# Kernel tuning notes

Hardware: AMD Instinct MI355X
Metric: run time of the kernel (lower is better)

The kernel has to match this reference:

```python
import jax, jax.numpy as jnp
import numpy as np

NUM_HEADS = 8
B, S, D = 4, 2048, 512


def setup_inputs() -> dict:
    key = jax.random.key(0)
    ks = jax.random.split(key, 12)
    scale = 1.0 / np.sqrt(D)
    return {
        "v": jax.random.normal(ks[0], (B, S, D), dtype=jnp.float32),
        "k": jax.random.normal(ks[1], (B, S, D), dtype=jnp.float32),
        "q": jax.random.normal(ks[2], (B, S, D), dtype=jnp.float32),
        "Wq": jax.random.normal(ks[3], (D, D), dtype=jnp.float32) * scale,
        "bq": jnp.zeros((D,), dtype=jnp.float32),
        "Wk": jax.random.normal(ks[4], (D, D), dtype=jnp.float32) * scale,
        "bk": jnp.zeros((D,), dtype=jnp.float32),
        "Wv": jax.random.normal(ks[5], (D, D), dtype=jnp.float32) * scale,
        "bv": jnp.zeros((D,), dtype=jnp.float32),
        "Wo": jax.random.normal(ks[6], (D, D), dtype=jnp.float32) * scale,
        "bo": jnp.zeros((D,), dtype=jnp.float32),
        "top_k": 32,
    }


def reference(v, k, q, Wq, bq, Wk, bk, Wv, bv, Wo, bo, top_k):
    dh = D // NUM_HEADS  # per-head depth

    def split_heads(x):  # [B,S,D] -> [B,H,S,dh]
        return x.reshape(B, -1, NUM_HEADS, dh).transpose(0, 2, 1, 3)

    qh = split_heads(q @ Wq + bq)
    kh = split_heads(k @ Wk + bk)
    vh = split_heads(v @ Wv + bv)

    logits = jnp.einsum('bhqd,bhkd->bhqk', qh, kh) / jnp.sqrt(jnp.float32(dh))
    w = jax.nn.softmax(logits, axis=-1)  # [B,H,S,S]

    num_keys = w.shape[-1]
    if top_k < num_keys:
        vals, idx = jax.lax.top_k(w, top_k)  # [B,H,S,top_k]
        bb = jnp.arange(B)[:, None, None, None]
        hh = jnp.arange(NUM_HEADS)[None, :, None, None]
        qq = jnp.arange(S)[None, None, :, None]
        sparse = jnp.zeros_like(w).at[bb, hh, qq, idx].set(vals)
        # tf.linalg.normalize(ord=1): divide by L1 norm along last axis
        w = sparse / jnp.sum(jnp.abs(sparse), axis=-1, keepdims=True)

    attn = jnp.einsum('bhqk,bhkd->bhqd', w, vh)  # [B,H,S,dh]
    concat = attn.transpose(0, 2, 1, 3).reshape(B, -1, D)
    out = concat @ Wo + bo
    return (out, w)
```

## Files before the change

### kernel.cpp

```cpp
#include <hip/hip_runtime.h>
#include <hip/hip_bf16.h>
#include <stdint.h>

#define S_LEN 2048
#define DMODEL 512
#define NH 8
#define DH 64
#define TOPK 32
#define LO_SCALE 4096.0f
#define INV_LO (1.0f/4096.0f)

typedef _Float16 f16;
typedef f16 half8 __attribute__((ext_vector_type(8)));
typedef f16 half4 __attribute__((ext_vector_type(4)));
typedef float floatx4 __attribute__((ext_vector_type(4)));
typedef float f32x4 __attribute__((ext_vector_type(4)));
typedef unsigned long long u64k;

#define AS1 __attribute__((address_space(1)))
#define AS3 __attribute__((address_space(3)))

__device__ __forceinline__ void gl_lds16(const void* g, void* l) {
    __builtin_amdgcn_global_load_lds((const AS1 void*)g, (AS3 void*)l, 16, 0, 0);
}
__device__ __forceinline__ void lds_fence() {
    asm volatile("s_waitcnt lgkmcnt(0)" ::: "memory");
}

__device__ __forceinline__ u64k make_key(float f, int idx) {
    unsigned u = __float_as_uint(f);
    unsigned sv = u ^ ((unsigned)(((int)u) >> 31) | 0x80000000u);
    return ((u64k)sv << 16) | (u64k)(0xFFFFu - (unsigned)idx);
}

__global__ __launch_bounds__(256)
void qkproj(const float* __restrict__ Xq, const float* __restrict__ Xk,
            const float* __restrict__ Wq_, const float* __restrict__ Wk_,
            const float* __restrict__ bq_, const float* __restrict__ bk_,
            float* __restrict__ outQ, float* __restrict__ outK)
{
    __shared__ float As[32][132];
    __shared__ float Bs[32][132];
    const float* X    = blockIdx.z ? Xk  : Xq;
    const float* W    = blockIdx.z ? Wk_ : Wq_;
    const float* bias = blockIdx.z ? bk_ : bq_;
    float* out        = blockIdx.z ? outK : outQ;
    const int tid = threadIdx.x;
    const int tx = tid & 15;
    const int ty = tid >> 4;
    const int m0 = blockIdx.y * 128;
    const int n0 = blockIdx.x * 128;

    float acc[8][8];
#pragma unroll
    for (int i = 0; i < 8; ++i)
#pragma unroll
        for (int j = 0; j < 8; ++j) acc[i][j] = 0.f;

    f32x4 pa[4], pb[4];
#pragma unroll
    for (int u = 0; u < 4; ++u) {
        int id = tid + u * 256;
        pa[u] = *(const f32x4*)(X + (size_t)(m0 + (id >> 3)) * 512 + (id & 7) * 4);
        pb[u] = *(const f32x4*)(W + (size_t)(id >> 5) * 512 + n0 + (id & 31) * 4);
    }

    for (int k0 = 0; k0 < 512; k0 += 32) {
#pragma unroll
        for (int u = 0; u < 4; ++u) {
            int id = tid + u * 256;
            int r = id >> 3, c4 = (id & 7) * 4;
            As[c4 + 0][r] = pa[u].x; As[c4 + 1][r] = pa[u].y;
            As[c4 + 2][r] = pa[u].z; As[c4 + 3][r] = pa[u].w;
            int rb = id >> 5, cb = (id & 31) * 4;
            *(f32x4*)&Bs[rb][cb] = pb[u];
        }
        __syncthreads();
        if (k0 < 480) {
            int kn = k0 + 32;
#pragma unroll
            for (int u = 0; u < 4; ++u) {
                int id = tid + u * 256;
                pa[u] = *(const f32x4*)(X + (size_t)(m0 + (id >> 3)) * 512 + kn + (id & 7) * 4);
                pb[u] = *(const f32x4*)(W + (size_t)(kn + (id >> 5)) * 512 + n0 + (id & 31) * 4);
            }
        }
#pragma unroll 8
        for (int kk = 0; kk < 32; ++kk) {
            float a[8], b[8];
            *(f32x4*)&a[0] = *(const f32x4*)&As[kk][ty * 4];
            *(f32x4*)&a[4] = *(const f32x4*)&As[kk][64 + ty * 4];
            *(f32x4*)&b[0] = *(const f32x4*)&Bs[kk][tx * 4];
            *(f32x4*)&b[4] = *(const f32x4*)&Bs[kk][64 + tx * 4];
#pragma unroll
            for (int i = 0; i < 8; ++i)
#pragma unroll
                for (int j = 0; j < 8; ++j)
                    acc[i][j] = fmaf(a[i], b[j], acc[i][j]);
        }
        __syncthreads();
    }

    float bb[8];
    *(f32x4*)&bb[0] = *(const f32x4*)(bias + n0 + tx * 4);
    *(f32x4*)&bb[4] = *(const f32x4*)(bias + n0 + 64 + tx * 4);

#pragma unroll
    for (int i = 0; i < 8; ++i) {
        int r = m0 + ((i >> 2) << 6) + ty * 4 + (i & 3);
        int b_ = r >> 11, s = r & 2047;
#pragma unroll
        for (int h = 0; h < 2; ++h) {
            int c = n0 + h * 64 + tx * 4;
            f32x4 w = {acc[i][h * 4 + 0] + bb[h * 4 + 0],
                       acc[i][h * 4 + 1] + bb[h * 4 + 1],
                       acc[i][h * 4 + 2] + bb[h * 4 + 2],
                       acc[i][h * 4 + 3] + bb[h * 4 + 3]};
            int hd = c >> 6, d = c & 63;
            float* p = out + (((size_t)(b_ * NH + hd) * S_LEN) + s) * DH + d;
            *(f32x4*)p = w;
        }
    }
}

__global__ __launch_bounds__(256)
void logits_topk(const float* __restrict__ Qh, const float* __restrict__ Kh,
                 float* __restrict__ wbuf)
{
    __shared__ float As[2][32][68];
    __shared__ __align__(16) char smemB[33280];
    float* Bs = (float*)smemB;
    u64k (*slab)[32] = (u64k(*)[32])smemB;

    const int tid = threadIdx.x;
    const int lig = tid & 15;
    const int ty  = tid >> 4;
    const int gsh = ((tid & 63) >> 4) << 4;
    const unsigned ltg = (1u << lig) - 1u;
    const int bh = blockIdx.y;
    const int q0 = blockIdx.x * 64;
    const float* Ab = Qh + (size_t)bh * S_LEN * DH;
    const float* Bb = Kh + (size_t)bh * S_LEN * DH;

    auto sort32 = [&](u64k &a0, u64k &a1) {
#pragma unroll
        for (int s = 2; s <= 32; s <<= 1) {
#pragma unroll
            for (int d = s >> 1; d >= 1; d >>= 1) {
                int e0 = 2 * lig;
                if (d == 1) {
                    bool descB = ((e0 & s) == 0);
                    u64k mx = a0 > a1 ? a0 : a1;
                    u64k mn = a0 > a1 ? a1 : a0;
                    a0 = descB ? mx : mn;
                    a1 = descB ? mn : mx;
                } else {
                    bool descB = ((e0 & s) == 0);
                    bool amS   = ((e0 & d) == 0);
                    bool wantMax = (descB == amS);
                    u64k p0 = __shfl_xor(a0, d >> 1, 16);
                    u64k p1 = __shfl_xor(a1, d >> 1, 16);
                    a0 = wantMax ? (a0 > p0 ? a0 : p0) : (a0 > p0 ? p0 : a0);
                    a1 = wantMax ? (a1 > p1 ? a1 : p1) : (a1 > p1 ? p1 : a1);
                }
            }
        }
    };
    auto clean32 = [&](u64k &a0, u64k &a1) {
#pragma unroll
        for (int d = 16; d >= 2; d >>= 1) {
            bool amS = (((2 * lig) & d) == 0);
            u64k p0 = __shfl_xor(a0, d >> 1, 16);
            u64k p1 = __shfl_xor(a1, d >> 1, 16);
            a0 = amS ? (a0 > p0 ? a0 : p0) : (a0 > p0 ? p0 : a0);
            a1 = amS ? (a1 > p1 ? a1 : p1) : (a1 > p1 ? p1 : a1);
        }
        u64k mx = a0 > a1 ? a0 : a1;
        u64k mn = a0 > a1 ? a1 : a0;
        a0 = mx; a1 = mn;
    };

    float acc[4][16];
#pragma unroll
    for (int i = 0; i < 4; ++i)
#pragma unroll
        for (int j = 0; j < 16; ++j) acc[i][j] = 0.f;

    u64k key0[4], key1[4], botk[4];
#pragma unroll
    for (int i = 0; i < 4; ++i) { key0[i] = 0; key1[i] = 0; botk[i] = 0; }

#pragma unroll
    for (int u = 0; u < 4; ++u) {
        int id = tid + u * 256;
        int r = id >> 4, c4 = (id & 15) * 4;
        int ch = c4 >> 5, cl = c4 & 31;
        f32x4 x = *(const f32x4*)(Ab + (size_t)(q0 + r) * DH + c4);
        As[ch][cl + 0][r] = x.x * 0.125f;
        As[ch][cl + 1][r] = x.y * 0.125f;
        As[ch][cl + 2][r] = x.z * 0.125f;
        As[ch][cl + 3][r] = x.w * 0.125f;
    }

    f32x4 kb[8];
#pragma unroll
    for (int u = 0; u < 8; ++u) {
        int id = tid + u * 256;
        int r = id >> 3, c4 = (id & 7) * 4;
        kb[u] = *(const f32x4*)(Bb + (size_t)r * DH + c4);
    }

#pragma unroll 1
    for (int kp = 0; kp < 8; ++kp) {
#pragma unroll
        for (int ch = 0; ch < 2; ++ch) {
            __syncthreads();
#pragma unroll
            for (int u = 0; u < 8; ++u) {
                int id = tid + u * 256;
                int r = id >> 3, c4 = (id & 7) * 4;
                Bs[(c4 + 0) * 260 + r] = kb[u].x;
                Bs[(c4 + 1) * 260 + r] = kb[u].y;
                Bs[(c4 + 2) * 260 + r] = kb[u].z;
                Bs[(c4 + 3) * 260 + r] = kb[u].w;
            }
            __syncthreads();
            {
                int nkp = ch ? kp + 1 : kp;
                int nch = ch ^ 1;
                if (nkp < 8) {
#pragma unroll
                    for (int u = 0; u < 8; ++u) {
                        int id = tid + u * 256;
                        int r = id >> 3, c4 = (id & 7) * 4;
                        kb[u] = *(const f32x4*)(Bb + (size_t)(nkp * 256 + r) * DH + nch * 32 + c4);
                    }
                }
            }
#pragma unroll 8
            for (int kk = 0; kk < 32; ++kk) {
                float a[4], b[16];
                *(f32x4*)&a[0] = *(const f32x4*)&As[ch][kk][ty * 4];
#pragma unroll
                for (int h = 0; h < 4; ++h)
                    *(f32x4*)&b[h * 4] = *(const f32x4*)&Bs[kk * 260 + lig * 4 + h * 64];
#pragma unroll
                for (int i = 0; i < 4; ++i)
#pragma unroll
                    for (int j = 0; j < 16; ++j)
                        acc[i][j] = fmaf(a[i], b[j], acc[i][j]);
            }
        }
        __syncthreads();

#pragma unroll
        for (int i = 0; i < 4; ++i) {
            unsigned done = 0;
            if (kp == 0) {
                u64k t0 = 0, t1 = 0; int j0 = 0, j1 = 0;
#pragma unroll
                for (int j = 0; j < 16; ++j) {
                    u64k kj = make_key(acc[i][j], ((j >> 2) << 6) + (lig << 2) + (j & 3));
                    if (kj > t0)      { t1 = t0; j1 = j0; t0 = kj; j0 = j; }
                    else if (kj > t1) { t1 = kj; j1 = j; }
                }
                key0[i] = t0; key1[i] = t1;
                sort32(key0[i], key1[i]);
                botk[i] = __shfl(key1[i], 15, 16);
                done = (1u << j0) | (1u << j1);
            }
            u64k bk = botk[i];
            int c = 0;
#pragma unroll 1
            for (int att = 0; att < 12; ++att) {
                bool ovf = false;
#pragma unroll
                for (int j = 0; j < 16; ++j) {
                    u64k kj = make_key(acc[i][j],
                                       kp * 256 + ((j >> 2) << 6) + (lig << 2) + (j & 3));
                    bool p = (((done >> j) & 1u) == 0u) && (kj > bk);
                    unsigned long long wbm = __ballot(p);
                    unsigned mk = (unsigned)((wbm >> gsh) & 0xFFFFull);
                    if (mk) {
                        int pos = c + __popc(mk & ltg);
                        int tot = c + __popc(mk);
                        if (p && pos < 32) { slab[ty * 4 + i][pos] = kj; done |= 1u << j; }
                        if (tot > 32) { ovf = true; c = 32; } else { c = tot; }
                    }
                }
                bool anyovf = __any(ovf);
                if (anyovf) {
                    lds_fence();
                    u64k c0 = (2 * lig     < c) ? slab[ty * 4 + i][2 * lig]     : 0ull;
                    u64k c1 = (2 * lig + 1 < c) ? slab[ty * 4 + i][2 * lig + 1] : 0ull;
                    sort32(c0, c1);
                    u64k m0 = __shfl_xor(c1, 15, 16);
                    u64k m1 = __shfl_xor(c0, 15, 16);
                    key0[i] = key0[i] > m0 ? key0[i] : m0;
                    key1[i] = key1[i] > m1 ? key1[i] : m1;
                    clean32(key0[i], key1[i]);
                    bk = __shfl(key1[i], 15, 16);
                    c = 0;
                } else {
                    break;
                }
            }
            {
                lds_fence();
                u64k c0 = (2 * lig     < c) ? slab[ty * 4 + i][2 * lig]     : 0ull;
                u64k c1 = (2 * lig + 1 < c) ? slab[ty * 4 + i][2 * lig + 1] : 0ull;
                sort32(c0, c1);
                u64k m0 = __shfl_xor(c1, 15, 16);
                u64k m1 = __shfl_xor(c0, 15, 16);
                key0[i] = key0[i] > m0 ? key0[i] : m0;
                key1[i] = key1[i] > m1 ? key1[i] : m1;
                clean32(key0[i], key1[i]);
                bk = __shfl(key1[i], 15, 16);
            }
            botk[i] = bk;
        }

#pragma unroll
        for (int i = 0; i < 4; ++i)
#pragma unroll
            for (int j = 0; j < 16; ++j) acc[i][j] = 0.f;
    }

#pragma unroll
    for (int i = 0; i < 4; ++i) {
        int r = q0 + ty * 4 + i;
        float* wr = wbuf + ((size_t)bh * S_LEN + r) * S_LEN;
        *(u64k*)(wr + (lig << 2))     = key0[i];
        *(u64k*)(wr + (lig << 2) + 2) = key1[i];
    }
}

__global__ __launch_bounds__(256)
void wsplit2(const float* __restrict__ W0, const float* __restrict__ W1,
             f16* __restrict__ planes)
{
    __shared__ float tile[32][33];
    const float* W = blockIdx.z ? W1 : W0;
    f16* Th = planes + (size_t)blockIdx.z * 524288;
    f16* Tl = Th + 262144;
    const int bx = blockIdx.x * 32;
    const int by = blockIdx.y * 32;
    const int lx = threadIdx.x & 31, ly = threadIdx.x >> 5;
#pragma unroll
    for (int r = ly; r < 32; r += 8)
        tile[r][lx] = W[(size_t)(by + r) * 512 + bx + lx];
    __syncthreads();
#pragma unroll
    for (int r = ly; r < 32; r += 8) {
        float x = tile[lx][r];
        f16 h = (f16)x;
        f16 l = (f16)((x - (float)h) * LO_SCALE);
        Th[(size_t)(bx + r) * 512 + by + lx] = h;
        Tl[(size_t)(bx + r) * 512 + by + lx] = l;
    }
}

__global__ __launch_bounds__(256)
void gemm_x32(const float* __restrict__ X,
              const f16* __restrict__ Bh_, const f16* __restrict__ Bl_,
              const float* __restrict__ bias, float* __restrict__ outF, int mode)
{
    __shared__ f16 sm[16384];
    f16* As_h = sm;       f16* As_l = sm + 4096;
    f16* Bs_h = sm + 8192; f16* Bs_l = sm + 12288;
    const int tid  = threadIdx.x;
    const int lane = tid & 63, wv = tid >> 6;
    const int wm = wv & 1, wn = wv >> 1;
    const int quad = lane >> 4, l15 = lane & 15;
    const int m0 = blockIdx.y * 128, n0 = blockIdx.x * 128;

    floatx4 acc_h[4][4], acc_c[4][4];
    const floatx4 z4 = {0.f, 0.f, 0.f, 0.f};
#pragma unroll
    for (int i = 0; i < 4; ++i)
#pragma unroll
        for (int j = 0; j < 4; ++j) { acc_h[i][j] = z4; acc_c[i][j] = z4; }

    for (int k0 = 0; k0 < 512; k0 += 32) {
        __syncthreads();
#pragma unroll
        for (int c = 0; c < 4; ++c) {
            int r   = c * 32 + (tid >> 3);
            int col = (tid & 7) * 4;
            f32x4 x = *(const f32x4*)(X + (size_t)(m0 + r) * 512 + k0 + col);
            f16 h0 = (f16)x.x, h1 = (f16)x.y, h2 = (f16)x.z, h3 = (f16)x.w;
            half4 hv = {h0, h1, h2, h3};
            half4 lv = {(f16)((x.x - (float)h0) * LO_SCALE),
                        (f16)((x.y - (float)h1) * LO_SCALE),
                        (f16)((x.z - (float)h2) * LO_SCALE),
                        (f16)((x.w - (float)h3) * LO_SCALE)};
            *(half4*)&As_h[r * 32 + col] = hv;
            *(half4*)&As_l[r * 32 + col] = lv;
        }
#pragma unroll
        for (int c = 0; c < 2; ++c) {
            int r    = c * 64 + (wv << 4) + (lane >> 2);
            int ch   = (lane & 3) * 8;
            int lidx = (c * 64 + (wv << 4)) * 32 + lane * 8;
            gl_lds16(Bh_ + (size_t)(n0 + r) * 512 + k0 + ch, &Bs_h[lidx]);
            gl_lds16(Bl_ + (size_t)(n0 + r) * 512 + k0 + ch, &Bs_l[lidx]);
        }
        asm volatile("s_waitcnt vmcnt(0)" ::: "memory");
        __syncthreads();

        half8 bh8[4], bl8[4];
#pragma unroll
        for (int j = 0; j < 4; ++j) {
            int n = wn * 64 + j * 16 + l15;
            bh8[j] = *(const half8*)&Bs_h[n * 32 + quad * 8];
            bl8[j] = *(const half8*)&Bs_l[n * 32 + quad * 8];
        }
#pragma unroll
        for (int i = 0; i < 4; ++i) {
            int m = wm * 64 + i * 16 + l15;
            half8 ah = *(const half8*)&As_h[m * 32 + quad * 8];
            half8 al = *(const half8*)&As_l[m * 32 + quad * 8];
#pragma unroll
            for (int j = 0; j < 4; ++j) {
                acc_h[i][j] = __builtin_amdgcn_mfma_f32_16x16x32_f16(ah, bh8[j], acc_h[i][j], 0, 0, 0);
                acc_c[i][j] = __builtin_amdgcn_mfma_f32_16x16x32_f16(ah, bl8[j], acc_c[i][j], 0, 0, 0);
                acc_c[i][j] = __builtin_amdgcn_mfma_f32_16x16x32_f16(al, bh8[j], acc_c[i][j], 0, 0, 0);
            }
        }
    }

#pragma unroll
    for (int j = 0; j < 4; ++j) {
        int col = n0 + wn * 64 + j * 16 + l15;
        float bv = bias[col];
#pragma unroll
        for (int i = 0; i < 4; ++i) {
            int rbase = m0 + wm * 64 + i * 16 + quad * 4;
#pragma unroll
            for (int rg = 0; rg < 4; ++rg) {
                float r = acc_h[i][j][rg] + acc_c[i][j][rg] * INV_LO + bv;
                int row = rbase + rg;
                if (mode == 2) {
                    outF[(size_t)row * 512 + col] = r;
                } else {
                    int b_ = row >> 11, s = row & 2047, h = col >> 6, d = col & 63;
                    outF[(((size_t)(b_ * NH + h)) * S_LEN + s) * DH + d] = r;
                }
            }
        }
    }
}

__global__ __launch_bounds__(256)
void gemm_x16(const f16* __restrict__ Ah_, const f16* __restrict__ Al_,
              const f16* __restrict__ Bh_, const f16* __restrict__ Bl_,
              const float* __restrict__ bias, float* __restrict__ outF,
              int Ksz, int ldc, int mode)
{
    __shared__ f16 sm[16384];
    f16* As_h = sm;        f16* As_l = sm + 4096;
    f16* Bs_h = sm + 8192; f16* Bs_l = sm + 12288;
    const int tid  = threadIdx.x;
    const int lane = tid & 63, wv = tid >> 6;
    const int wm = wv & 1, wn = wv >> 1;
    const int quad = lane >> 4, l15 = lane & 15;
    const int m0 = blockIdx.y * 128, n0 = blockIdx.x * 128;

    floatx4 acc_h[4][4], acc_c[4][4];
    const floatx4 z4 = {0.f, 0.f, 0.f, 0.f};
#pragma unroll
    for (int i = 0; i < 4; ++i)
#pragma unroll
        for (int j = 0; j < 4; ++j) { acc_h[i][j] = z4; acc_c[i][j] = z4; }

    for (int k0 = 0; k0 < Ksz; k0 += 32) {
        __syncthreads();
#pragma unroll
        for (int c = 0; c < 2; ++c) {
            int r    = c * 64 + (wv << 4) + (lane >> 2);
            int ch   = (lane & 3) * 8;
            int lidx = (c * 64 + (wv << 4)) * 32 + lane * 8;
            gl_lds16(Ah_ + (size_t)(m0 + r) * Ksz + k0 + ch, &As_h[lidx]);
            gl_lds16(Al_ + (size_t)(m0 + r) * Ksz + k0 + ch, &As_l[lidx]);
            gl_lds16(Bh_ + (size_t)(n0 + r) * Ksz + k0 + ch, &Bs_h[lidx]);
            gl_lds16(Bl_ + (size_t)(n0 + r) * Ksz + k0 + ch, &Bs_l[lidx]);
        }
        asm volatile("s_waitcnt vmcnt(0)" ::: "memory");
        __syncthreads();

        half8 bh8[4], bl8[4];
#pragma unroll
        for (int j = 0; j < 4; ++j) {
            int n = wn * 64 + j * 16 + l15;
            bh8[j] = *(const half8*)&Bs_h[n * 32 + quad * 8];
            bl8[j] = *(const half8*)&Bs_l[n * 32 + quad * 8];
        }
#pragma unroll
        for (int i = 0; i < 4; ++i) {
            int m = wm * 64 + i * 16 + l15;
            half8 ah = *(const half8*)&As_h[m * 32 + quad * 8];
            half8 al = *(const half8*)&As_l[m * 32 + quad * 8];
#pragma unroll
            for (int j = 0; j < 4; ++j) {
                acc_h[i][j] = __builtin_amdgcn_mfma_f32_16x16x32_f16(ah, bh8[j], acc_h[i][j], 0, 0, 0);
                acc_c[i][j] = __builtin_amdgcn_mfma_f32_16x16x32_f16(ah, bl8[j], acc_c[i][j], 0, 0, 0);
                acc_c[i][j] = __builtin_amdgcn_mfma_f32_16x16x32_f16(al, bh8[j], acc_c[i][j], 0, 0, 0);
            }
        }
    }

#pragma unroll
    for (int j = 0; j < 4; ++j) {
        int col = n0 + wn * 64 + j * 16 + l15;
        float bv = (mode == 2) ? bias[col] : 0.f;
#pragma unroll
        for (int i = 0; i < 4; ++i) {
            int rbase = m0 + wm * 64 + i * 16 + quad * 4;
#pragma unroll
            for (int rg = 0; rg < 4; ++rg) {
                float r = acc_h[i][j][rg] + acc_c[i][j][rg] * INV_LO;
                int row = rbase + rg;
                outF[(size_t)row * ldc + col] = r + bv;
            }
        }
    }
}

__global__ __launch_bounds__(256)
void topk_scatter(float* __restrict__ wbuf, const float* __restrict__ Vh,
                  f16* __restrict__ attH, f16* __restrict__ attL)
{
    __shared__ float wrow[4][2048];
    __shared__ float win_w[4][TOPK];
    __shared__ int   win_i[4][TOPK];

    const int tid  = threadIdx.x;
    const int wv   = tid >> 6;
    const int lane = tid & 63;
    const int row  = blockIdx.x * 4 + wv;
    float* wr = wbuf + (size_t)row * 2048;

    u64k key = 0;
    if (lane < TOPK) key = ((const u64k*)wr)[lane];
    unsigned sv = (unsigned)(key >> 16);
    unsigned fu = (sv & 0x80000000u) ? (sv ^ 0x80000000u) : ~sv;
    float v = __uint_as_float(fu);
    int idx = (int)(0xFFFFu - (unsigned)(key & 0xFFFFull)) & 2047;

    float m = __shfl(v, 0, 64);
    float e = (lane < TOPK) ? __expf(v - m) : 0.f;

    float mysum = e;
#pragma unroll
    for (int off = 32; off > 0; off >>= 1) mysum += __shfl_xor(mysum, off, 64);
    const float rw = 1.f / mysum;

    if (lane < TOPK) { win_w[wv][lane] = e; win_i[wv][lane] = idx; }

    const f32x4 z = {0.f, 0.f, 0.f, 0.f};
#pragma unroll
    for (int t = 0; t < 8; ++t) ((f32x4*)wrow[wv])[t * 64 + lane] = z;
    lds_fence();
    if (lane < TOPK) wrow[wv][win_i[wv][lane]] = win_w[wv][lane] * rw;
    lds_fence();

#pragma unroll
    for (int t = 0; t < 8; ++t)
        __builtin_nontemporal_store(((f32x4*)wrow[wv])[t * 64 + lane],
                                    (f32x4*)(wr + (size_t)(t * 64 + lane) * 4));

    const int bh = row >> 11;
    const float* Vb = Vh + (size_t)bh * S_LEN * DH;
    float acc = 0.f;
#pragma unroll
    for (int j = 0; j < TOPK; ++j) {
        float wj = win_w[wv][j] * rw;
        int   kj = win_i[wv][j];
        acc = fmaf(wj, Vb[(size_t)kj * DH + lane], acc);
    }
    const int b_ = row >> 14;
    const int h  = (row >> 11) & 7;
    const int s  = row & 2047;
    size_t oidx = (((size_t)b_ * S_LEN) + s) * 512 + h * DH + lane;
    f16 hh = (f16)acc;
    attH[oidx] = hh;
    attL[oidx] = (f16)((acc - (float)hh) * LO_SCALE);
}

extern "C" void kernel_launch(void* const* d_in, const int* in_sizes, int n_in,
                              void* d_out, int out_size, void* d_ws, size_t ws_size,
                              hipStream_t stream) {
    const float* v  = (const float*)d_in[0];
    const float* k  = (const float*)d_in[1];
    const float* q  = (const float*)d_in[2];
    const float* Wq = (const float*)d_in[3];
    const float* bq = (const float*)d_in[4];
    const float* Wk = (const float*)d_in[5];
    const float* bk = (const float*)d_in[6];
    const float* Wv = (const float*)d_in[7];
    const float* bv = (const float*)d_in[8];
    const float* Wo = (const float*)d_in[9];
    const float* bo = (const float*)d_in[10];

    float* out  = (float*)d_out;
    float* wout = out + (size_t)4 * S_LEN * 512;

    char* ws = (char*)d_ws;
    float* Vh   = (float*)ws;
    float* Qh32 = (float*)(ws + 16777216);
    float* Kh32 = (float*)(ws + 33554432);
    f16* WT  = (f16*)(ws + 50331648);
    f16 *WvH = WT,           *WvL = WT + 262144;
    f16 *WoH = WT + 524288,  *WoL = WT + 786432;
    f16* attH = (f16*)(ws + 16777216);
    f16* attL = (f16*)(ws + 25165824);

    wsplit2<<<dim3(16, 16, 2), 256, 0, stream>>>(Wv, Wo, WT);

    qkproj<<<dim3(4, 64, 2), 256, 0, stream>>>(q, k, Wq, Wk, bq, bk, Qh32, Kh32);
    gemm_x32<<<dim3(4, 64), 256, 0, stream>>>(v, WvH, WvL, bv, Vh, 1);

    logits_topk<<<dim3(32, 32), 256, 0, stream>>>(Qh32, Kh32, wout);

    topk_scatter<<<16384, 256, 0, stream>>>(wout, Vh, attH, attL);

    gemm_x16<<<dim3(4, 64, 1), 256, 0, stream>>>(attH, attL, WoH, WoL, bo, out, 512, 512, 2);
}
```

Measured before the change: 1.194 ms.

## Split fused logits+topk into full logits GEMM and per-row topk attention kernel

Replaces the fused kernel, which computed logits and tracked the top-k candidates in registers across eight key passes, with two kernels. The first is a tiled FP32 GEMM that writes the full logits matrix into the weight output buffer. The second runs one wavefront per row: it reads the row back, selects the top-k with a 64-lane bitonic sort plus threshold filtering, and then does the scatter and attention. This gives much more parallelism and removes per-pass selection from the GEMM loop, at the cost of writing and then re-reading the full B*H*S*S logits through HBM.

```diff
diff --git a/kernel.cpp b/kernel.cpp
--- a/kernel.cpp
+++ b/kernel.cpp
@@ -123,31 +123,311 @@
     }
 }
 
-__global__ __launch_bounds__(256)
-void logits_topk(const float* __restrict__ Qh, const float* __restrict__ Kh,
-                 float* __restrict__ wbuf)
+__global__ __launch_bounds__(256, 2)
+void gemm_logits(const float* __restrict__ Qh, const float* __restrict__ Kh,
+                 float* __restrict__ logits)
 {
-    __shared__ float As[2][32][68];
-    __shared__ __align__(16) char smemB[33280];
-    float* Bs = (float*)smemB;
-    u64k (*slab)[32] = (u64k(*)[32])smemB;
-
+    __shared__ float As[32][132];
+    __shared__ float Bs[32][260];
     const int tid = threadIdx.x;
-    const int lig = tid & 15;
-    const int ty  = tid >> 4;
-    const int gsh = ((tid & 63) >> 4) << 4;
-    const unsigned ltg = (1u << lig) - 1u;
-    const int bh = blockIdx.y;
-    const int q0 = blockIdx.x * 64;
+    const int tx = tid & 15;
+    const int ty = tid >> 4;
+    const int bh = blockIdx.z;
     const float* Ab = Qh + (size_t)bh * S_LEN * DH;
     const float* Bb = Kh + (size_t)bh * S_LEN * DH;
+    const int q0 = blockIdx.y * 128;
+    const int k0 = blockIdx.x * 256;
+
+    float acc[8][16];
+#pragma unroll
+    for (int i = 0; i < 8; ++i)
+#pragma unroll
+        for (int j = 0; j < 16; ++j) acc[i][j] = 0.f;
+
+    f32x4 qa[4], kb[8];
+#pragma unroll
+    for (int u = 0; u < 4; ++u) {
+        int id = tid + u * 256;
+        qa[u] = *(const f32x4*)(Ab + (size_t)(q0 + (id >> 3)) * DH + (id & 7) * 4);
+    }
+#pragma unroll
+    for (int u = 0; u < 8; ++u) {
+        int id = tid + u * 256;
+        kb[u] = *(const f32x4*)(Bb + (size_t)(k0 + (id >> 3)) * DH + (id & 7) * 4);
+    }
+
+    for (int ch = 0; ch < 2; ++ch) {
+#pragma unroll
+        for (int u = 0; u < 4; ++u) {
+            int id = tid + u * 256;
+            int r = id >> 3, c4 = (id & 7) * 4;
+            As[c4 + 0][r] = qa[u].x * 0.125f; As[c4 + 1][r] = qa[u].y * 0.125f;
+            As[c4 + 2][r] = qa[u].z * 0.125f; As[c4 + 3][r] = qa[u].w * 0.125f;
+        }
+#pragma unroll
+        for (int u = 0; u < 8; ++u) {
+            int id = tid + u * 256;
+            int r = id >> 3, c4 = (id & 7) * 4;
+            Bs[c4 + 0][r] = kb[u].x; Bs[c4 + 1][r] = kb[u].y;
+            Bs[c4 + 2][r] = kb[u].z; Bs[c4 + 3][r] = kb[u].w;
+        }
+        __syncthreads();
+        if (ch == 0) {
+#pragma unroll
+            for (int u = 0; u < 4; ++u) {
+                int id = tid + u * 256;
+                qa[u] = *(const f32x4*)(Ab + (size_t)(q0 + (id >> 3)) * DH + 32 + (id & 7) * 4);
+            }
+#pragma unroll
+            for (int u = 0; u < 8; ++u) {
+                int id = tid + u * 256;
+                kb[u] = *(const f32x4*)(Bb + (size_t)(k0 + (id >> 3)) * DH + 32 + (id & 7) * 4);
+            }
+        }
+#pragma unroll 8
+        for (int kk = 0; kk < 32; ++kk) {
+            float a[8], b[16];
+            *(f32x4*)&a[0] = *(const f32x4*)&As[kk][ty * 4];
+            *(f32x4*)&a[4] = *(const f32x4*)&As[kk][64 + ty * 4];
+#pragma unroll
+            for (int h = 0; h < 4; ++h)
+                *(f32x4*)&b[h * 4] = *(const f32x4*)&Bs[kk][tx * 4 + h * 64];
+#pragma unroll
+            for (int i = 0; i < 8; ++i)
+#pragma unroll
+                for (int j = 0; j < 16; ++j)
+                    acc[i][j] = fmaf(a[i], b[j], acc[i][j]);
+        }
+        __syncthreads();
+    }
+
+#pragma unroll
+    for (int i = 0; i < 8; ++i) {
+        int r = q0 + (i >> 2) * 64 + ty * 4 + (i & 3);
+        float* C = logits + (size_t)bh * S_LEN * S_LEN + (size_t)r * S_LEN + k0;
+#pragma unroll
+        for (int h = 0; h < 4; ++h) {
+            f32x4 v = {acc[i][h * 4 + 0], acc[i][h * 4 + 1],
+                       acc[i][h * 4 + 2], acc[i][h * 4 + 3]};
+            __builtin_nontemporal_store(v, (f32x4*)(C + h * 64 + tx * 4));
+        }
+    }
+}
+
+__global__ __launch_bounds__(256)
+void wsplit2(const float* __restrict__ W0, const float* __restrict__ W1,
+             f16* __restrict__ planes)
+{
+    __shared__ float tile[32][33];
+    const float* W = blockIdx.z ? W1 : W0;
+    f16* Th = planes + (size_t)blockIdx.z * 524288;
+    f16* Tl = Th + 262144;
+    const int bx = blockIdx.x * 32;
+    const int by = blockIdx.y * 32;
+    const int lx = threadIdx.x & 31, ly = threadIdx.x >> 5;
+#pragma unroll
+    for (int r = ly; r < 32; r += 8)
+        tile[r][lx] = W[(size_t)(by + r) * 512 + bx + lx];
+    __syncthreads();
+#pragma unroll
+    for (int r = ly; r < 32; r += 8) {
+        float x = tile[lx][r];
+        f16 h = (f16)x;
+        f16 l = (f16)((x - (float)h) * LO_SCALE);
+        Th[(size_t)(bx + r) * 512 + by + lx] = h;
+        Tl[(size_t)(bx + r) * 512 + by + lx] = l;
+    }
+}
+
+__global__ __launch_bounds__(256)
+void gemm_x32(const float* __restrict__ X,
+              const f16* __restrict__ Bh_, const f16* __restrict__ Bl_,
+              const float* __restrict__ bias, float* __restrict__ outF, int mode)
+{
+    __shared__ f16 sm[16384];
+    f16* As_h = sm;       f16* As_l = sm + 4096;
+    f16* Bs_h = sm + 8192; f16* Bs_l = sm + 12288;
+    const int tid  = threadIdx.x;
+    const int lane = tid & 63, wv = tid >> 6;
+    const int wm = wv & 1, wn = wv >> 1;
+    const int quad = lane >> 4, l15 = lane & 15;
+    const int m0 = blockIdx.y * 128, n0 = blockIdx.x * 128;
+
+    floatx4 acc_h[4][4], acc_c[4][4];
+    const floatx4 z4 = {0.f, 0.f, 0.f, 0.f};
+#pragma unroll
+    for (int i = 0; i < 4; ++i)
+#pragma unroll
+        for (int j = 0; j < 4; ++j) { acc_h[i][j] = z4; acc_c[i][j] = z4; }
+
+    for (int k0 = 0; k0 < 512; k0 += 32) {
+        __syncthreads();
+#pragma unroll
+        for (int c = 0; c < 4; ++c) {
+            int r   = c * 32 + (tid >> 3);
+            int col = (tid & 7) * 4;
+            f32x4 x = *(const f32x4*)(X + (size_t)(m0 + r) * 512 + k0 + col);
+            f16 h0 = (f16)x.x, h1 = (f16)x.y, h2 = (f16)x.z, h3 = (f16)x.w;
+            half4 hv = {h0, h1, h2, h3};
+            half4 lv = {(f16)((x.x - (float)h0) * LO_SCALE),
+                        (f16)((x.y - (float)h1) * LO_SCALE),
+                        (f16)((x.z - (float)h2) * LO_SCALE),
+                        (f16)((x.w - (float)h3) * LO_SCALE)};
+            *(half4*)&As_h[r * 32 + col] = hv;
+            *(half4*)&As_l[r * 32 + col] = lv;
+        }
+#pragma unroll
+        for (int c = 0; c < 2; ++c) {
+            int r    = c * 64 + (wv << 4) + (lane >> 2);
+            int ch   = (lane & 3) * 8;
+            int lidx = (c * 64 + (wv << 4)) * 32 + lane * 8;
+            gl_lds16(Bh_ + (size_t)(n0 + r) * 512 + k0 + ch, &Bs_h[lidx]);
+            gl_lds16(Bl_ + (size_t)(n0 + r) * 512 + k0 + ch, &Bs_l[lidx]);
+        }
+        asm volatile("s_waitcnt vmcnt(0)" ::: "memory");
+        __syncthreads();
+
+        half8 bh8[4], bl8[4];
+#pragma unroll
+        for (int j = 0; j < 4; ++j) {
+            int n = wn * 64 + j * 16 + l15;
+            bh8[j] = *(const half8*)&Bs_h[n * 32 + quad * 8];
+            bl8[j] = *(const half8*)&Bs_l[n * 32 + quad * 8];
+        }
+#pragma unroll
+        for (int i = 0; i < 4; ++i) {
+            int m = wm * 64 + i * 16 + l15;
+            half8 ah = *(const half8*)&As_h[m * 32 + quad * 8];
+            half8 al = *(const half8*)&As_l[m * 32 + quad * 8];
+#pragma unroll
+            for (int j = 0; j < 4; ++j) {
+                acc_h[i][j] = __builtin_amdgcn_mfma_f32_16x16x32_f16(ah, bh8[j], acc_h[i][j], 0, 0, 0);
+                acc_c[i][j] = __builtin_amdgcn_mfma_f32_16x16x32_f16(ah, bl8[j], acc_c[i][j], 0, 0, 0);
+                acc_c[i][j] = __builtin_amdgcn_mfma_f32_16x16x32_f16(al, bh8[j], acc_c[i][j], 0, 0, 0);
+            }
+        }
+    }
+
+#pragma unroll
+    for (int j = 0; j < 4; ++j) {
+        int col = n0 + wn * 64 + j * 16 + l15;
+        float bv = bias[col];
+#pragma unroll
+        for (int i = 0; i < 4; ++i) {
+            int rbase = m0 + wm * 64 + i * 16 + quad * 4;
+#pragma unroll
+            for (int rg = 0; rg < 4; ++rg) {
+                float r = acc_h[i][j][rg] + acc_c[i][j][rg] * INV_LO + bv;
+                int row = rbase + rg;
+                if (mode == 2) {
+                    outF[(size_t)row * 512 + col] = r;
+                } else {
+                    int b_ = row >> 11, s = row & 2047, h = col >> 6, d = col & 63;
+                    outF[(((size_t)(b_ * NH + h)) * S_LEN + s) * DH + d] = r;
+                }
+            }
+        }
+    }
+}
+
+__global__ __launch_bounds__(256)
+void gemm_x16(const f16* __restrict__ Ah_, const f16* __restrict__ Al_,
+              const f16* __restrict__ Bh_, const f16* __restrict__ Bl_,
+              const float* __restrict__ bias, float* __restrict__ outF,
+              int Ksz, int ldc, int mode)
+{
+    __shared__ f16 sm[16384];
+    f16* As_h = sm;        f16* As_l = sm + 4096;
+    f16* Bs_h = sm + 8192; f16* Bs_l = sm + 12288;
+    const int tid  = threadIdx.x;
+    const int lane = tid & 63, wv = tid >> 6;
+    const int wm = wv & 1, wn = wv >> 1;
+    const int quad = lane >> 4, l15 = lane & 15;
+    const int m0 = blockIdx.y * 128, n0 = blockIdx.x * 128;
+
+    floatx4 acc_h[4][4], acc_c[4][4];
+    const floatx4 z4 = {0.f, 0.f, 0.f, 0.f};
+#pragma unroll
+    for (int i = 0; i < 4; ++i)
+#pragma unroll
+        for (int j = 0; j < 4; ++j) { acc_h[i][j] = z4; acc_c[i][j] = z4; }
+
+    for (int k0 = 0; k0 < Ksz; k0 += 32) {
+        __syncthreads();
+#pragma unroll
+        for (int c = 0; c < 2; ++c) {
+            int r    = c * 64 + (wv << 4) + (lane >> 2);
+            int ch   = (lane & 3) * 8;
+            int lidx = (c * 64 + (wv << 4)) * 32 + lane * 8;
+            gl_lds16(Ah_ + (size_t)(m0 + r) * Ksz + k0 + ch, &As_h[lidx]);
+            gl_lds16(Al_ + (size_t)(m0 + r) * Ksz + k0 + ch, &As_l[lidx]);
+            gl_lds16(Bh_ + (size_t)(n0 + r) * Ksz + k0 + ch, &Bs_h[lidx]);
+            gl_lds16(Bl_ + (size_t)(n0 + r) * Ksz + k0 + ch, &Bs_l[lidx]);
+        }
+        asm volatile("s_waitcnt vmcnt(0)" ::: "memory");
+        __syncthreads();
+
+        half8 bh8[4], bl8[4];
+#pragma unroll
+        for (int j = 0; j < 4; ++j) {
+            int n = wn * 64 + j * 16 + l15;
+            bh8[j] = *(const half8*)&Bs_h[n * 32 + quad * 8];
+            bl8[j] = *(const half8*)&Bs_l[n * 32 + quad * 8];
+        }
+#pragma unroll
+        for (int i = 0; i < 4; ++i) {
+            int m = wm * 64 + i * 16 + l15;
+            half8 ah = *(const half8*)&As_h[m * 32 + quad * 8];
+            half8 al = *(const half8*)&As_l[m * 32 + quad * 8];
+#pragma unroll
+            for (int j = 0; j < 4; ++j) {
+                acc_h[i][j] = __builtin_amdgcn_mfma_f32_16x16x32_f16(ah, bh8[j], acc_h[i][j], 0, 0, 0);
+                acc_c[i][j] = __builtin_amdgcn_mfma_f32_16x16x32_f16(ah, bl8[j], acc_c[i][j], 0, 0, 0);
+                acc_c[i][j] = __builtin_amdgcn_mfma_f32_16x16x32_f16(al, bh8[j], acc_c[i][j], 0, 0, 0);
+            }
+        }
+    }
+
+#pragma unroll
+    for (int j = 0; j < 4; ++j) {
+        int col = n0 + wn * 64 + j * 16 + l15;
+        float bv = (mode == 2) ? bias[col] : 0.f;
+#pragma unroll
+        for (int i = 0; i < 4; ++i) {
+            int rbase = m0 + wm * 64 + i * 16 + quad * 4;
+#pragma unroll
+            for (int rg = 0; rg < 4; ++rg) {
+                float r = acc_h[i][j][rg] + acc_c[i][j][rg] * INV_LO;
+                int row = rbase + rg;
+                outF[(size_t)row * ldc + col] = r + bv;
+            }
+        }
+    }
+}
+
+__global__ __launch_bounds__(256)
+void topk_attn(float* __restrict__ wbuf, const float* __restrict__ Vh,
+               f16* __restrict__ attH, f16* __restrict__ attL)
+{
+    __shared__ float wrow[4][2048];
+    __shared__ u64k  slab[4][32];
+    __shared__ float win_w[4][TOPK];
+    __shared__ int   win_i[4][TOPK];
+
+    const int tid  = threadIdx.x;
+    const int wv   = tid >> 6;
+    const int lane = tid & 63;
+    const int l15  = lane & 15;
+    const unsigned long long lt = (1ull << lane) - 1ull;
+    const int row = blockIdx.x * 4 + wv;
+    float* wr = wbuf + (size_t)row * 2048;
 
     auto sort32 = [&](u64k &a0, u64k &a1) {
 #pragma unroll
         for (int s = 2; s <= 32; s <<= 1) {
 #pragma unroll
             for (int d = s >> 1; d >= 1; d >>= 1) {
-                int e0 = 2 * lig;
+                int e0 = 2 * l15;
                 if (d == 1) {
                     bool descB = ((e0 & s) == 0);
                     u64k mx = a0 > a1 ? a0 : a1;
@@ -169,7 +449,7 @@
     auto clean32 = [&](u64k &a0, u64k &a1) {
 #pragma unroll
         for (int d = 16; d >= 2; d >>= 1) {
-            bool amS = (((2 * lig) & d) == 0);
+            bool amS = (((2 * l15) & d) == 0);
             u64k p0 = __shfl_xor(a0, d >> 1, 16);
             u64k p1 = __shfl_xor(a1, d >> 1, 16);
             a0 = amS ? (a0 > p0 ? a0 : p0) : (a0 > p0 ? p0 : a0);
@@ -179,369 +459,102 @@
         u64k mn = a0 > a1 ? a1 : a0;
         a0 = mx; a1 = mn;
     };
-
-    float acc[4][16];
-#pragma unroll
-    for (int i = 0; i < 4; ++i)
-#pragma unroll
-        for (int j = 0; j < 16; ++j) acc[i][j] = 0.f;
-
-    u64k key0[4], key1[4], botk[4];
-#pragma unroll
-    for (int i = 0; i < 4; ++i) { key0[i] = 0; key1[i] = 0; botk[i] = 0; }
-
-#pragma unroll
-    for (int u = 0; u < 4; ++u) {
-        int id = tid + u * 256;
-        int r = id >> 4, c4 = (id & 15) * 4;
-        int ch = c4 >> 5, cl = c4 & 31;
-        f32x4 x = *(const f32x4*)(Ab + (size_t)(q0 + r) * DH + c4);
-        As[ch][cl + 0][r] = x.x * 0.125f;
-        As[ch][cl + 1][r] = x.y * 0.125f;
-        As[ch][cl + 2][r] = x.z * 0.125f;
-        As[ch][cl + 3][r] = x.w * 0.125f;
-    }
-
-    f32x4 kb[8];
-#pragma unroll
-    for (int u = 0; u < 8; ++u) {
-        int id = tid + u * 256;
-        int r = id >> 3, c4 = (id & 7) * 4;
-        kb[u] = *(const f32x4*)(Bb + (size_t)r * DH + c4);
-    }
-
+    auto sort128 = [&](u64k &a0, u64k &a1) {
+#pragma unroll
+        for (int s = 2; s <= 128; s <<= 1) {
+#pragma unroll
+            for (int d = s >> 1; d >= 1; d >>= 1) {
+                int e0 = 2 * lane;
+                if (d == 1) {
+                    bool descB = ((e0 & s) == 0);
+                    u64k mx = a0 > a1 ? a0 : a1;
+                    u64k mn = a0 > a1 ? a1 : a0;
+                    a0 = descB ? mx : mn;
+                    a1 = descB ? mn : mx;
+                } else {
+                    bool descB = ((e0 & s) == 0);
+                    bool amS   = ((e0 & d) == 0);
+                    bool wantMax = (descB == amS);
+                    u64k p0 = __shfl_xor(a0, d >> 1, 64);
+                    u64k p1 = __shfl_xor(a1, d >> 1, 64);
+                    a0 = wantMax ? (a0 > p0 ? a0 : p0) : (a0 > p0 ? p0 : a0);
+                    a1 = wantMax ? (a1 > p1 ? a1 : p1) : (a1 > p1 ? p1 : a1);
+                }
+            }
+        }
+    };
+
+    float L[32];
+#pragma unroll
+    for (int t = 0; t < 8; ++t) {
+        f32x4 x = __builtin_nontemporal_load((const f32x4*)(wr + t * 256 + lane * 4));
+        L[4 * t + 0] = x.x; L[4 * t + 1] = x.y; L[4 * t + 2] = x.z; L[4 * t + 3] = x.w;
+    }
+
+    const f32x4 z = {0.f, 0.f, 0.f, 0.f};
+#pragma unroll
+    for (int t = 0; t < 8; ++t) ((f32x4*)wrow[wv])[t * 64 + lane] = z;
+
+    u64k k0 = 0, k1 = 0; int j0 = 0, j1 = 0;
+#pragma unroll
+    for (int u = 0; u < 32; ++u) {
+        u64k kj = make_key(L[u], ((u >> 2) << 8) + (lane << 2) + (u & 3));
+        if (kj > k0)      { k1 = k0; j1 = j0; k0 = kj; j0 = u; }
+        else if (kj > k1) { k1 = kj; j1 = u; }
+    }
+    sort128(k0, k1);
+    u64k bk = __shfl(k1, 15, 64);
+
+    unsigned done = (1u << j0) | (1u << j1);
+    int c = 0;
 #pragma unroll 1
-    for (int kp = 0; kp < 8; ++kp) {
-#pragma unroll
-        for (int ch = 0; ch < 2; ++ch) {
-            __syncthreads();
-#pragma unroll
-            for (int u = 0; u < 8; ++u) {
-                int id = tid + u * 256;
-                int r = id >> 3, c4 = (id & 7) * 4;
-                Bs[(c4 + 0) * 260 + r] = kb[u].x;
-                Bs[(c4 + 1) * 260 + r] = kb[u].y;
-                Bs[(c4 + 2) * 260 + r] = kb[u].z;
-                Bs[(c4 + 3) * 260 + r] = kb[u].w;
-            }
-            __syncthreads();
-            {
-                int nkp = ch ? kp + 1 : kp;
-                int nch = ch ^ 1;
-                if (nkp < 8) {
-#pragma unroll
-                    for (int u = 0; u < 8; ++u) {
-                        int id = tid + u * 256;
-                        int r = id >> 3, c4 = (id & 7) * 4;
-                        kb[u] = *(const f32x4*)(Bb + (size_t)(nkp * 256 + r) * DH + nch * 32 + c4);
-                    }
-                }
-            }
-#pragma unroll 8
-            for (int kk = 0; kk < 32; ++kk) {
-                float a[4], b[16];
-                *(f32x4*)&a[0] = *(const f32x4*)&As[ch][kk][ty * 4];
-#pragma unroll
-                for (int h = 0; h < 4; ++h)
-                    *(f32x4*)&b[h * 4] = *(const f32x4*)&Bs[kk * 260 + lig * 4 + h * 64];
-#pragma unroll
-                for (int i = 0; i < 4; ++i)
-#pragma unroll
-                    for (int j = 0; j < 16; ++j)
-                        acc[i][j] = fmaf(a[i], b[j], acc[i][j]);
-            }
-        }
-        __syncthreads();
-
-#pragma unroll
-        for (int i = 0; i < 4; ++i) {
-            unsigned done = 0;
-            if (kp == 0) {
-                u64k t0 = 0, t1 = 0; int j0 = 0, j1 = 0;
-#pragma unroll
-                for (int j = 0; j < 16; ++j) {
-                    u64k kj = make_key(acc[i][j], ((j >> 2) << 6) + (lig << 2) + (j & 3));
-                    if (kj > t0)      { t1 = t0; j1 = j0; t0 = kj; j0 = j; }
-                    else if (kj > t1) { t1 = kj; j1 = j; }
-                }
-                key0[i] = t0; key1[i] = t1;
-                sort32(key0[i], key1[i]);
-                botk[i] = __shfl(key1[i], 15, 16);
-                done = (1u << j0) | (1u << j1);
-            }
-            u64k bk = botk[i];
-            int c = 0;
-#pragma unroll 1
-            for (int att = 0; att < 12; ++att) {
-                bool ovf = false;
-#pragma unroll
-                for (int j = 0; j < 16; ++j) {
-                    u64k kj = make_key(acc[i][j],
-                                       kp * 256 + ((j >> 2) << 6) + (lig << 2) + (j & 3));
-                    bool p = (((done >> j) & 1u) == 0u) && (kj > bk);
-                    unsigned long long wbm = __ballot(p);
-                    unsigned mk = (unsigned)((wbm >> gsh) & 0xFFFFull);
-                    if (mk) {
-                        int pos = c + __popc(mk & ltg);
-                        int tot = c + __popc(mk);
-                        if (p && pos < 32) { slab[ty * 4 + i][pos] = kj; done |= 1u << j; }
-                        if (tot > 32) { ovf = true; c = 32; } else { c = tot; }
-                    }
-                }
-                bool anyovf = __any(ovf);
-                if (anyovf) {
-                    lds_fence();
-                    u64k c0 = (2 * lig     < c) ? slab[ty * 4 + i][2 * lig]     : 0ull;
-                    u64k c1 = (2 * lig + 1 < c) ? slab[ty * 4 + i][2 * lig + 1] : 0ull;
-                    sort32(c0, c1);
-                    u64k m0 = __shfl_xor(c1, 15, 16);
-                    u64k m1 = __shfl_xor(c0, 15, 16);
-                    key0[i] = key0[i] > m0 ? key0[i] : m0;
-                    key1[i] = key1[i] > m1 ? key1[i] : m1;
-                    clean32(key0[i], key1[i]);
-                    bk = __shfl(key1[i], 15, 16);
-                    c = 0;
-                } else {
-                    break;
-                }
-            }
-            {
-                lds_fence();
-                u64k c0 = (2 * lig     < c) ? slab[ty * 4 + i][2 * lig]     : 0ull;
-                u64k c1 = (2 * lig + 1 < c) ? slab[ty * 4 + i][2 * lig + 1] : 0ull;
-                sort32(c0, c1);
-                u64k m0 = __shfl_xor(c1, 15, 16);
-                u64k m1 = __shfl_xor(c0, 15, 16);
-                key0[i] = key0[i] > m0 ? key0[i] : m0;
-                key1[i] = key1[i] > m1 ? key1[i] : m1;
-                clean32(key0[i], key1[i]);
-                bk = __shfl(key1[i], 15, 16);
-            }
-            botk[i] = bk;
-        }
-
-#pragma unroll
-        for (int i = 0; i < 4; ++i)
-#pragma unroll
-            for (int j = 0; j < 16; ++j) acc[i][j] = 0.f;
-    }
-
-#pragma unroll
-    for (int i = 0; i < 4; ++i) {
-        int r = q0 + ty * 4 + i;
-        float* wr = wbuf + ((size_t)bh * S_LEN + r) * S_LEN;
-        *(u64k*)(wr + (lig << 2))     = key0[i];
-        *(u64k*)(wr + (lig << 2) + 2) = key1[i];
-    }
-}
-
-__global__ __launch_bounds__(256)
-void wsplit2(const float* __restrict__ W0, const float* __restrict__ W1,
-             f16* __restrict__ planes)
-{
-    __shared__ float tile[32][33];
-    const float* W = blockIdx.z ? W1 : W0;
-    f16* Th = planes + (size_t)blockIdx.z * 524288;
-    f16* Tl = Th + 262144;
-    const int bx = blockIdx.x * 32;
-    const int by = blockIdx.y * 32;
-    const int lx = threadIdx.x & 31, ly = threadIdx.x >> 5;
-#pragma unroll
-    for (int r = ly; r < 32; r += 8)
-        tile[r][lx] = W[(size_t)(by + r) * 512 + bx + lx];
-    __syncthreads();
-#pragma unroll
-    for (int r = ly; r < 32; r += 8) {
-        float x = tile[lx][r];
-        f16 h = (f16)x;
-        f16 l = (f16)((x - (float)h) * LO_SCALE);
-        Th[(size_t)(bx + r) * 512 + by + lx] = h;
-        Tl[(size_t)(bx + r) * 512 + by + lx] = l;
-    }
-}
-
-__global__ __launch_bounds__(256)
-void gemm_x32(const float* __restrict__ X,
-              const f16* __restrict__ Bh_, const f16* __restrict__ Bl_,
-              const float* __restrict__ bias, float* __restrict__ outF, int mode)
-{
-    __shared__ f16 sm[16384];
-    f16* As_h = sm;       f16* As_l = sm + 4096;
-    f16* Bs_h = sm + 8192; f16* Bs_l = sm + 12288;
-    const int tid  = threadIdx.x;
-    const int lane = tid & 63, wv = tid >> 6;
-    const int wm = wv & 1, wn = wv >> 1;
-    const int quad = lane >> 4, l15 = lane & 15;
-    const int m0 = blockIdx.y * 128, n0 = blockIdx.x * 128;
-
-    floatx4 acc_h[4][4], acc_c[4][4];
-    const floatx4 z4 = {0.f, 0.f, 0.f, 0.f};
-#pragma unroll
-    for (int i = 0; i < 4; ++i)
-#pragma unroll
-        for (int j = 0; j < 4; ++j) { acc_h[i][j] = z4; acc_c[i][j] = z4; }
-
-    for (int k0 = 0; k0 < 512; k0 += 32) {
-        __syncthreads();
-#pragma unroll
-        for (int c = 0; c < 4; ++c) {
-            int r   = c * 32 + (tid >> 3);
-            int col = (tid & 7) * 4;
-            f32x4 x = *(const f32x4*)(X + (size_t)(m0 + r) * 512 + k0 + col);
-            f16 h0 = (f16)x.x, h1 = (f16)x.y, h2 = (f16)x.z, h3 = (f16)x.w;
-            half4 hv = {h0, h1, h2, h3};
-            half4 lv = {(f16)((x.x - (float)h0) * LO_SCALE),
-                        (f16)((x.y - (float)h1) * LO_SCALE),
-                        (f16)((x.z - (float)h2) * LO_SCALE),
-                        (f16)((x.w - (float)h3) * LO_SCALE)};
-            *(half4*)&As_h[r * 32 + col] = hv;
-            *(half4*)&As_l[r * 32 + col] = lv;
-        }
-#pragma unroll
-        for (int c = 0; c < 2; ++c) {
-            int r    = c * 64 + (wv << 4) + (lane >> 2);
-            int ch   = (lane & 3) * 8;
-            int lidx = (c * 64 + (wv << 4)) * 32 + lane * 8;
-            gl_lds16(Bh_ + (size_t)(n0 + r) * 512 + k0 + ch, &Bs_h[lidx]);
-            gl_lds16(Bl_ + (size_t)(n0 + r) * 512 + k0 + ch, &Bs_l[lidx]);
-        }
-        asm volatile("s_waitcnt vmcnt(0)" ::: "memory");
-        __syncthreads();
-
-        half8 bh8[4], bl8[4];
-#pragma unroll
-        for (int j = 0; j < 4; ++j) {
-            int n = wn * 64 + j * 16 + l15;
-            bh8[j] = *(const half8*)&Bs_h[n * 32 + quad * 8];
-            bl8[j] = *(const half8*)&Bs_l[n * 32 + quad * 8];
-        }
-#pragma unroll
-        for (int i = 0; i < 4; ++i) {
-            int m = wm * 64 + i * 16 + l15;
-            half8 ah = *(const half8*)&As_h[m * 32 + quad * 8];
-            half8 al = *(const half8*)&As_l[m * 32 + quad * 8];
-#pragma unroll
-            for (int j = 0; j < 4; ++j) {
-                acc_h[i][j] = __builtin_amdgcn_mfma_f32_16x16x32_f16(ah, bh8[j], acc_h[i][j], 0, 0, 0);
-                acc_c[i][j] = __builtin_amdgcn_mfma_f32_16x16x32_f16(ah, bl8[j], acc_c[i][j], 0, 0, 0);
-                acc_c[i][j] = __builtin_amdgcn_mfma_f32_16x16x32_f16(al, bh8[j], acc_c[i][j], 0, 0, 0);
-            }
-        }
-    }
-
-#pragma unroll
-    for (int j = 0; j < 4; ++j) {
-        int col = n0 + wn * 64 + j * 16 + l15;
-        float bv = bias[col];
-#pragma unroll
-        for (int i = 0; i < 4; ++i) {
-            int rbase = m0 + wm * 64 + i * 16 + quad * 4;
-#pragma unroll
-            for (int rg = 0; rg < 4; ++rg) {
-                float r = acc_h[i][j][rg] + acc_c[i][j][rg] * INV_LO + bv;
-                int row = rbase + rg;
-                if (mode == 2) {
-                    outF[(size_t)row * 512 + col] = r;
-                } else {
-                    int b_ = row >> 11, s = row & 2047, h = col >> 6, d = col & 63;
-                    outF[(((size_t)(b_ * NH + h)) * S_LEN + s) * DH + d] = r;
-                }
-            }
-        }
-    }
-}
-
-__global__ __launch_bounds__(256)
-void gemm_x16(const f16* __restrict__ Ah_, const f16* __restrict__ Al_,
-              const f16* __restrict__ Bh_, const f16* __restrict__ Bl_,
-              const float* __restrict__ bias, float* __restrict__ outF,
-              int Ksz, int ldc, int mode)
-{
-    __shared__ f16 sm[16384];
-    f16* As_h = sm;        f16* As_l = sm + 4096;
-    f16* Bs_h = sm + 8192; f16* Bs_l = sm + 12288;
-    const int tid  = threadIdx.x;
-    const int lane = tid & 63, wv = tid >> 6;
-    const int wm = wv & 1, wn = wv >> 1;
-    const int quad = lane >> 4, l15 = lane & 15;
-    const int m0 = blockIdx.y * 128, n0 = blockIdx.x * 128;
-
-    floatx4 acc_h[4][4], acc_c[4][4];
-    const floatx4 z4 = {0.f, 0.f, 0.f, 0.f};
-#pragma unroll
-    for (int i = 0; i < 4; ++i)
-#pragma unroll
-        for (int j = 0; j < 4; ++j) { acc_h[i][j] = z4; acc_c[i][j] = z4; }
-
-    for (int k0 = 0; k0 < Ksz; k0 += 32) {
-        __syncthreads();
-#pragma unroll
-        for (int c = 0; c < 2; ++c) {
-            int r    = c * 64 + (wv << 4) + (lane >> 2);
-            int ch   = (lane & 3) * 8;
-            int lidx = (c * 64 + (wv << 4)) * 32 + lane * 8;
-            gl_lds16(Ah_ + (size_t)(m0 + r) * Ksz + k0 + ch, &As_h[lidx]);
-            gl_lds16(Al_ + (size_t)(m0 + r) * Ksz + k0 + ch, &As_l[lidx]);
-            gl_lds16(Bh_ + (size_t)(n0 + r) * Ksz + k0 + ch, &Bs_h[lidx]);
-            gl_lds16(Bl_ + (size_t)(n0 + r) * Ksz + k0 + ch, &Bs_l[lidx]);
-        }
-        asm volatile("s_waitcnt vmcnt(0)" ::: "memory");
-        __syncthreads();
-
-        half8 bh8[4], bl8[4];
-#pragma unroll
-        for (int j = 0; j < 4; ++j) {
-            int n = wn * 64 + j * 16 + l15;
-            bh8[j] = *(const half8*)&Bs_h[n * 32 + quad * 8];
-            bl8[j] = *(const half8*)&Bs_l[n * 32 + quad * 8];
-        }
-#pragma unroll
-        for (int i = 0; i < 4; ++i) {
-            int m = wm * 64 + i * 16 + l15;
-            half8 ah = *(const half8*)&As_h[m * 32 + quad * 8];
-            half8 al = *(const half8*)&As_l[m * 32 + quad * 8];
-#pragma unroll
-            for (int j = 0; j < 4; ++j) {
-                acc_h[i][j] = __builtin_amdgcn_mfma_f32_16x16x32_f16(ah, bh8[j], acc_h[i][j], 0, 0, 0);
-                acc_c[i][j] = __builtin_amdgcn_mfma_f32_16x16x32_f16(ah, bl8[j], acc_c[i][j], 0, 0, 0);
-                acc_c[i][j] = __builtin_amdgcn_mfma_f32_16x16x32_f16(al, bh8[j], acc_c[i][j], 0, 0, 0);
-            }
-        }
-    }
-
-#pragma unroll
-    for (int j = 0; j < 4; ++j) {
-        int col = n0 + wn * 64 + j * 16 + l15;
-        float bv = (mode == 2) ? bias[col] : 0.f;
-#pragma unroll
-        for (int i = 0; i < 4; ++i) {
-            int rbase = m0 + wm * 64 + i * 16 + quad * 4;
-#pragma unroll
-            for (int rg = 0; rg < 4; ++rg) {
-                float r = acc_h[i][j][rg] + acc_c[i][j][rg] * INV_LO;
-                int row = rbase + rg;
-                outF[(size_t)row * ldc + col] = r + bv;
-            }
-        }
-    }
-}
-
-__global__ __launch_bounds__(256)
-void topk_scatter(float* __restrict__ wbuf, const float* __restrict__ Vh,
-                  f16* __restrict__ attH, f16* __restrict__ attL)
-{
-    __shared__ float wrow[4][2048];
-    __shared__ float win_w[4][TOPK];
-    __shared__ int   win_i[4][TOPK];
-
-    const int tid  = threadIdx.x;
-    const int wv   = tid >> 6;
-    const int lane = tid & 63;
-    const int row  = blockIdx.x * 4 + wv;
-    float* wr = wbuf + (size_t)row * 2048;
-
-    u64k key = 0;
-    if (lane < TOPK) key = ((const u64k*)wr)[lane];
+    for (int att = 0; att < 70; ++att) {
+        bool ovf = false;
+#pragma unroll 4
+        for (int u = 0; u < 32; ++u) {
+            u64k kj = make_key(L[u], ((u >> 2) << 8) + (lane << 2) + (u & 3));
+            bool p = (((done >> u) & 1u) == 0u) && (kj > bk);
+            unsigned long long mk = __ballot(p);
+            if (mk) {
+                int pos = c + (int)__popcll(mk & lt);
+                int tot = c + (int)__popcll(mk);
+                if (p && pos < 32) { slab[wv][pos] = kj; done |= 1u << u; }
+                if (tot > 32) { ovf = true; c = 32; } else { c = tot; }
+            }
+        }
+        bool anyovf = __any(ovf);
+        if (anyovf) {
+            lds_fence();
+            u64k c0 = (2 * l15     < c) ? slab[wv][2 * l15]     : 0ull;
+            u64k c1 = (2 * l15 + 1 < c) ? slab[wv][2 * l15 + 1] : 0ull;
+            sort32(c0, c1);
+            u64k m0 = __shfl_xor(c1, 15, 16);
+            u64k m1 = __shfl_xor(c0, 15, 16);
+            k0 = k0 > m0 ? k0 : m0;
+            k1 = k1 > m1 ? k1 : m1;
+            clean32(k0, k1);
+            bk = __shfl(k1, 15, 64);
+            c = 0;
+        } else {
+            break;
+        }
+    }
+    {
+        lds_fence();
+        u64k c0 = (2 * l15     < c) ? slab[wv][2 * l15]     : 0ull;
+        u64k c1 = (2 * l15 + 1 < c) ? slab[wv][2 * l15 + 1] : 0ull;
+        sort32(c0, c1);
+        u64k m0 = __shfl_xor(c1, 15, 16);
+        u64k m1 = __shfl_xor(c0, 15, 16);
+        k0 = k0 > m0 ? k0 : m0;
+        k1 = k1 > m1 ? k1 : m1;
+        clean32(k0, k1);
+    }
+
+    if (lane < 16) { slab[wv][2 * lane] = k0; slab[wv][2 * lane + 1] = k1; }
+    lds_fence();
+
+    u64k key = (lane < TOPK) ? slab[wv][lane] : 0ull;
     unsigned sv = (unsigned)(key >> 16);
     unsigned fu = (sv & 0x80000000u) ? (sv ^ 0x80000000u) : ~sv;
     float v = __uint_as_float(fu);
@@ -556,10 +569,6 @@
     const float rw = 1.f / mysum;
 
     if (lane < TOPK) { win_w[wv][lane] = e; win_i[wv][lane] = idx; }
-
-    const f32x4 z = {0.f, 0.f, 0.f, 0.f};
-#pragma unroll
-    for (int t = 0; t < 8; ++t) ((f32x4*)wrow[wv])[t * 64 + lane] = z;
     lds_fence();
     if (lane < TOPK) wrow[wv][win_i[wv][lane]] = win_w[wv][lane] * rw;
     lds_fence();
@@ -620,9 +629,9 @@
     qkproj<<<dim3(4, 64, 2), 256, 0, stream>>>(q, k, Wq, Wk, bq, bk, Qh32, Kh32);
     gemm_x32<<<dim3(4, 64), 256, 0, stream>>>(v, WvH, WvL, bv, Vh, 1);
 
-    logits_topk<<<dim3(32, 32), 256, 0, stream>>>(Qh32, Kh32, wout);
-
-    topk_scatter<<<16384, 256, 0, stream>>>(wout, Vh, attH, attL);
+    gemm_logits<<<dim3(8, 16, 32), 256, 0, stream>>>(Qh32, Kh32, wout);
+
+    topk_attn<<<16384, 256, 0, stream>>>(wout, Vh, attH, attL);
 
     gemm_x16<<<dim3(4, 64, 1), 256, 0, stream>>>(attH, attL, WoH, WoL, bo, out, 512, 512, 2);
 }
```

Result: faster. 1.157 ms (-3.2%).
